# Kernel optimization log

Hardware: AMD Instinct MI355X
Metric: run time of the kernel (lower is better)

## Reference

```python
import jax, jax.numpy as jnp
import numpy as np

N_HEAD = 16


def setup_inputs() -> dict:
    key = jax.random.key(0)
    k1, k2, k3 = jax.random.split(key, 3)
    B, S, D = 4, 2048, 1024
    scale = 1.0 / np.sqrt(D)
    return {
        "inp": jax.random.normal(k1, (B, S, D), dtype=jnp.float32),
        "w_attn": jax.random.normal(k2, (D, 3 * D), dtype=jnp.float32) * scale,
        "b_attn": jnp.zeros((3 * D,), dtype=jnp.float32),
        "w_proj": jax.random.normal(k3, (D, D), dtype=jnp.float32) * scale,
        "b_proj": jnp.zeros((D,), dtype=jnp.float32),
    }


def reference(inp, w_attn, b_attn, w_proj, b_proj):
    B, S, D = inp.shape
    H = N_HEAD
    hd = D // H
    qkv = inp @ w_attn + b_attn                      # [B,S,3D]
    q, k, v = jnp.split(qkv, 3, axis=-1)
    q = q.reshape(B, S, H, hd)
    k = k.reshape(B, S, H, hd)
    v = v.reshape(B, S, H, hd)
    # scores [B,H,S,S], scaled by 1/sqrt(head_dim)
    scores = jnp.einsum("bqhd,bkhd->bhqk", q, k) / jnp.sqrt(jnp.asarray(hd, dtype=inp.dtype))
    # causal mask: position q attends to k <= q
    causal = jnp.tril(jnp.ones((S, S), dtype=bool))
    scores = jnp.where(causal[None, None], scores, jnp.asarray(-jnp.inf, dtype=scores.dtype))
    probs = jax.nn.softmax(scores, axis=-1)          # dropout omitted (eval mode)
    ctx = jnp.einsum("bhqk,bkhd->bqhd", probs, v).reshape(B, S, D)
    return ctx @ w_proj + b_proj
```

## Files before the change

### kernel.cpp

```cpp
#include <hip/hip_runtime.h>


#define DEV __device__ __forceinline__

typedef unsigned short u16;
typedef u16   u16x8 __attribute__((ext_vector_type(8)));
typedef u16   u16x4 __attribute__((ext_vector_type(4)));
typedef float f32x4v __attribute__((ext_vector_type(4)));
typedef __bf16 bf16x8 __attribute__((ext_vector_type(8)));

#define BB 4
#define SS 2048
#define DD 1024
#define HH 16
#define HD 64
#define MM (BB*SS)
#define N3D (3*DD)
#define C8  0.18033688011112042f

DEV u16 f2bf(float f) { return __builtin_bit_cast(u16, (__bf16)f); }
DEV float bf2f(u16 h) { return __builtin_bit_cast(float, (unsigned)h << 16); }

DEV f32x4v mfma16(u16x8 a, u16x8 b, f32x4v c) {
  return __builtin_amdgcn_mfma_f32_16x16x32_bf16(
      __builtin_bit_cast(bf16x8, a), __builtin_bit_cast(bf16x8, b), c, 0, 0, 0);
}

DEV void async16(const void* g, void* l) {
  __builtin_amdgcn_global_load_lds(
      (const __attribute__((address_space(1))) void*)g,
      (__attribute__((address_space(3))) void*)l, 16, 0, 0);
}

template <int C> DEV float dpp_fmax(float x) {
  int xi = __builtin_bit_cast(int, x);
  int y = __builtin_amdgcn_update_dpp(xi, xi, C, 0xF, 0xF, false);
  return fmaxf(x, __builtin_bit_cast(float, y));
}
template <int C> DEV float dpp_fadd(float x) {
  int xi = __builtin_bit_cast(int, x);
  int y = __builtin_amdgcn_update_dpp(xi, xi, C, 0xF, 0xF, false);
  return x + __builtin_bit_cast(float, y);
}
DEV float rowmax16(float x) {
  x = dpp_fmax<0x121>(x);
  x = dpp_fmax<0x122>(x);
  x = dpp_fmax<0x124>(x);
  x = dpp_fmax<0x128>(x);
  return x;
}
DEV float rowsum16(float x) {
  x = dpp_fadd<0x121>(x);
  x = dpp_fadd<0x122>(x);
  x = dpp_fadd<0x124>(x);
  x = dpp_fadd<0x128>(x);
  return x;
}

__global__ __launch_bounds__(256) void prep_kernel(
    const float* __restrict__ inp, const float* __restrict__ w_attn,
    const float* __restrict__ w_proj, u16* __restrict__ Abf,
    u16* __restrict__ WAt, u16* __restrict__ WPt) {
  const int bid = blockIdx.x;
  const int tid = threadIdx.x;
  if (bid < 4096) {
    __shared__ float t[32][33];
    const float* W; u16* Wt; int N, K, n0, k0;
    if (bid < 3072) { W = w_attn; Wt = WAt; N = N3D; K = DD;
                      n0 = (bid % 96) * 32; k0 = (bid / 96) * 32; }
    else            { W = w_proj; Wt = WPt; N = DD;  K = DD;
                      int tb = bid - 3072; n0 = (tb % 32) * 32; k0 = (tb / 32) * 32; }
    int tx = tid & 31, ty = tid >> 5;
    for (int i = ty; i < 32; i += 8)
      t[i][tx] = W[(long long)(k0 + i) * N + n0 + tx];
    __syncthreads();
    for (int i = ty; i < 32; i += 8)
      Wt[(long long)(n0 + i) * K + k0 + tx] = f2bf(t[tx][i]);
  } else {
    const long long n = (long long)MM * DD;
    long long i = (long long)(bid - 4096) * 256 + tid;
    for (long long j = i * 4; j < n; j += 2048LL * 256 * 4) {
      f32x4v v = *(const f32x4v*)(inp + j);
      u16x4 o;
      o.x = f2bf(v.x); o.y = f2bf(v.y); o.z = f2bf(v.z); o.w = f2bf(v.w);
      *(u16x4*)(Abf + j) = o;
    }
  }
}

__global__ __launch_bounds__(256) void gemm_kernel(
    const u16* __restrict__ A, const u16* __restrict__ Bt,
    const float* __restrict__ bias, void* __restrict__ Cout,
    u16* __restrict__ Vt, int Ndim, int Kdim, int mode) {
  __shared__ __align__(16) char smem[65536];

  const int tid = threadIdx.x;
  const int lane = tid & 63, wid = tid >> 6;
  const int l15 = lane & 15, lg = lane >> 4;

  const int nwg = (int)(gridDim.x * gridDim.y);
  const int orig = (int)(blockIdx.y * gridDim.x + blockIdx.x);
  const int wg = (orig & 7) * (nwg >> 3) + (orig >> 3);
  const int bx = wg % (int)gridDim.x, by = wg / (int)gridDim.x;
  const int rb = by * 128, cb = bx * 128;
  const int wr = (wid >> 1) * 64, wc = (wid & 1) * 64;

  f32x4v acc[4][4] = {};

  const int rlo = tid >> 3;
  const int cbS = (tid & 7) * 16;
  const int swS = cbS ^ ((rlo & 7) << 4);
  const int sd  = rlo * 128 + cbS;

  const int xr  = (l15 & 7) << 4;
  const int vaA = l15 * 128 + ((lg * 16) ^ xr);
  const int gvA0 = wr * 128 + vaA, gvA1 = gvA0 ^ 64;
  const int gvB0 = wc * 128 + vaA, gvB1 = gvB0 ^ 64;

  const char* pa[4];
  const char* pb[4];
#pragma unroll
  for (int i = 0; i < 4; ++i) {
    pa[i] = (const char*)A  + (long long)(rb + i * 32 + rlo) * (Kdim * 2) + swS;
    pb[i] = (const char*)Bt + (long long)(cb + i * 32 + rlo) * (Kdim * 2) + swS;
  }

  auto stage = [&](int dofs, int kb) {
#pragma unroll
    for (int i = 0; i < 4; ++i) {
      async16(pa[i] + kb, smem + dofs + i * 4096 + sd);
      async16(pb[i] + kb, smem + 32768 + dofs + i * 4096 + sd);
    }
  };

  auto compute = [&](int aofs, int bofs) {
    u16x8 a0[4], b0[4], a1[4], b1[4];
#pragma unroll
    for (int mi = 0; mi < 4; ++mi) {
      a0[mi] = *(const u16x8*)(smem + aofs + mi * 2048 + gvA0);
      a1[mi] = *(const u16x8*)(smem + aofs + mi * 2048 + gvA1);
    }
#pragma unroll
    for (int ni = 0; ni < 4; ++ni) {
      b0[ni] = *(const u16x8*)(smem + bofs + ni * 2048 + gvB0);
      b1[ni] = *(const u16x8*)(smem + bofs + ni * 2048 + gvB1);
    }
#pragma unroll
    for (int mi = 0; mi < 4; ++mi)
#pragma unroll
      for (int ni = 0; ni < 4; ++ni) {
        acc[mi][ni] = mfma16(a0[mi], b0[ni], acc[mi][ni]);
        acc[mi][ni] = mfma16(a1[mi], b1[ni], acc[mi][ni]);
      }
  };

  const int nK = Kdim >> 6;
  stage(0, 0);
  __syncthreads();
  for (int kt = 0; kt < nK; kt += 2) {
    stage(16384, 128);
    compute(0, 32768);
    __syncthreads();
    if (kt + 2 < nK) stage(0, 256);
    compute(16384, 49152);
    __syncthreads();
#pragma unroll
    for (int i = 0; i < 4; ++i) { pa[i] += 256; pb[i] += 256; }
  }

#pragma unroll
  for (int mi = 0; mi < 4; ++mi)
#pragma unroll
    for (int ni = 0; ni < 4; ++ni) {
      int col = cb + wc + ni * 16 + l15;
      float bv = bias[col];
      if (mode == 1 && col >= 2 * DD) {
        int h = (col >> 6) & 15, d = col & 63;
#pragma unroll
        for (int r = 0; r < 4; ++r) {
          int row = rb + wr + mi * 16 + lg * 4 + r;
          int b = row >> 11, s = row & 2047;
          Vt[(((long long)(b * HH + h) * HD + d) << 11) + s] = f2bf(acc[mi][ni][r] + bv);
        }
      } else {
#pragma unroll
        for (int r = 0; r < 4; ++r) {
          int row = rb + wr + mi * 16 + lg * 4 + r;
          float v = acc[mi][ni][r] + bv;
          if (mode) ((u16*)Cout)[(long long)row * Ndim + col] = f2bf(v);
          else      ((float*)Cout)[(long long)row * Ndim + col] = v;
        }
      }
    }
}

__global__ __launch_bounds__(512, 4) void attn_kernel(
    const u16* __restrict__ qkv, const u16* __restrict__ Vt,
    u16* __restrict__ ctx) {
  __shared__ __align__(16) char smem[49152];

  const int tid = threadIdx.x, lane = tid & 63, wid = tid >> 6;
  const int l15 = lane & 15, lg = lane >> 4;

  const int orig = (int)blockIdx.x;
  const int wgid = (orig & 7) * 64 + (orig >> 3);
  const int pair = wgid & 7;
  const int bh = wgid >> 3;
  const int b = bh >> 4, h = bh & 15;

  const u16* Qcol = qkv + (long long)b * SS * N3D + h * HD;
  const u16* Kcol = qkv + (long long)b * SS * N3D + DD + h * HD;
  const u16* Vbh  = Vt + (long long)bh * HD * SS;

  const int xr  = (l15 & 7) << 4;
  const int vaA = l15 * 128 + ((lg * 16) ^ xr);
  const int vaB = vaA ^ 64;
  const int vpA = 32768 + wid * 2048 + vaA;
  const int vpB = vpA ^ 64;

  int pw[16];
#pragma unroll
  for (int r = 0; r < 4; ++r) {
    int row = lg * 4 + r;
#pragma unroll
    for (int ni = 0; ni < 4; ++ni)
      pw[r * 4 + ni] = 32768 + wid * 2048 + row * 128 +
                       (((ni * 16 + l15) * 2) ^ ((row & 7) << 4));
  }

  const int rlo = tid >> 3;
  const int cbS = (tid & 7) * 16;
  const int swS = cbS ^ ((rlo & 7) << 4);
  const int sd  = rlo * 128 + cbS;
  const long long KSTP = 64LL * N3D * 2;
  const long long VSTP = 64LL * 2;

  auto stage = [&](int dofs, const char* ka, const char* va) {
    async16(ka, smem + dofs + sd);
    async16(va, smem + 16384 + dofs + sd);
  };

#pragma unroll 1
  for (int half = 0; half < 2; ++half) {
    const int qt = half ? pair : 15 - pair;
    const int q0 = qt * 128;
    const int qw = q0 + wid * 16;
    const int nkb = 2 * qt + 2;

    u16x8 qf[2];
#pragma unroll
    for (int kk = 0; kk < 2; ++kk)
      qf[kk] = *(const u16x8*)(Qcol + (long long)(qw + l15) * N3D + kk * 32 + lg * 8);

    f32x4v acc[4] = {};
    float m_s[4], l_p[4];
#pragma unroll
    for (int r = 0; r < 4; ++r) { m_s[r] = -1e30f; l_p[r] = 0.f; }

    const char* ka = (const char*)Kcol + (long long)rlo * (N3D * 2) + swS;
    const char* va = (const char*)Vbh + (long long)rlo * (SS * 2) + swS;

    auto compute = [&](int kofs, int vofs, int kbase) {
      if (kbase > qw + 15) return;

      f32x4v s[4] = {};
      u16x8 bfr0[4], bfr1[4];
#pragma unroll
      for (int ni = 0; ni < 4; ++ni)
        bfr0[ni] = *(const u16x8*)(smem + kofs + ni * 2048 + vaA);
      __builtin_amdgcn_s_setprio(1);
#pragma unroll
      for (int ni = 0; ni < 4; ++ni)
        s[ni] = mfma16(qf[0], bfr0[ni], s[ni]);
      __builtin_amdgcn_s_setprio(0);
#pragma unroll
      for (int ni = 0; ni < 4; ++ni)
        bfr1[ni] = *(const u16x8*)(smem + kofs + ni * 2048 + vaB);
      __builtin_amdgcn_s_setprio(1);
#pragma unroll
      for (int ni = 0; ni < 4; ++ni)
        s[ni] = mfma16(qf[1], bfr1[ni], s[ni]);
      __builtin_amdgcn_s_setprio(0);

      if (kbase + 63 > qw) {
#pragma unroll
        for (int ni = 0; ni < 4; ++ni) {
          int kcol = kbase + ni * 16 + l15;
#pragma unroll
          for (int r = 0; r < 4; ++r) {
            int qrow = qw + lg * 4 + r;
            if (kcol > qrow) s[ni][r] = -1e30f;
          }
        }
      }

      float lmax[4];
      bool need = false;
#pragma unroll
      for (int r = 0; r < 4; ++r) {
        lmax[r] = fmaxf(fmaxf(fmaxf(s[0][r], s[1][r]), s[2][r]), s[3][r]);
        need = need || (lmax[r] > m_s[r] + 64.f);
      }
      if (__any(need)) {
#pragma unroll
        for (int r = 0; r < 4; ++r) {
          float rm = rowmax16(lmax[r]);
          float newm = fmaxf(m_s[r], rm);
          float sc = __builtin_exp2f((m_s[r] - newm) * C8);
          m_s[r] = newm;
          l_p[r] *= sc;
#pragma unroll
          for (int di = 0; di < 4; ++di) acc[di][r] *= sc;
        }
      }
#pragma unroll
      for (int r = 0; r < 4; ++r) {
        float mC = m_s[r] * C8;
        float rsum = 0.f;
#pragma unroll
        for (int ni = 0; ni < 4; ++ni) {
          float p = __builtin_exp2f(__builtin_fmaf(s[ni][r], C8, -mC));
          s[ni][r] = p;
          rsum += p;
        }
        l_p[r] += rsum;
      }

#pragma unroll
      for (int r = 0; r < 4; ++r)
#pragma unroll
        for (int ni = 0; ni < 4; ++ni)
          *(u16*)(smem + pw[r * 4 + ni]) = f2bf(s[ni][r]);

      u16x8 pa0 = *(const u16x8*)(smem + vpA);
      u16x8 pa1 = *(const u16x8*)(smem + vpB);
      u16x8 vb0[4], vb1[4];
#pragma unroll
      for (int di = 0; di < 4; ++di) {
        vb0[di] = *(const u16x8*)(smem + vofs + di * 2048 + vaA);
        vb1[di] = *(const u16x8*)(smem + vofs + di * 2048 + vaB);
      }
      __builtin_amdgcn_s_setprio(1);
#pragma unroll
      for (int di = 0; di < 4; ++di) {
        acc[di] = mfma16(pa0, vb0[di], acc[di]);
        acc[di] = mfma16(pa1, vb1[di], acc[di]);
      }
      __builtin_amdgcn_s_setprio(0);
    };

    stage(0, ka, va);
    __syncthreads();

    for (int kb = 0; kb < nkb; kb += 2) {
      stage(8192, ka + KSTP, va + VSTP);
      compute(0, 16384, kb * 64);
      __syncthreads();
      if (kb + 2 < nkb) stage(0, ka + 2 * KSTP, va + 2 * VSTP);
      compute(8192, 24576, (kb + 1) * 64);
      __syncthreads();
      ka += 2 * KSTP; va += 2 * VSTP;
    }

#pragma unroll
    for (int r = 0; r < 4; ++r) {
      float inv = 1.f / rowsum16(l_p[r]);
      int qrow = qw + lg * 4 + r;
#pragma unroll
      for (int di = 0; di < 4; ++di) {
        int d = di * 16 + l15;
        ctx[((long long)(b * SS + qrow)) * DD + h * HD + d] = f2bf(acc[di][r] * inv);
      }
    }
  }
}

extern "C" void kernel_launch(void* const* d_in, const int* in_sizes, int n_in,
                              void* d_out, int out_size, void* d_ws, size_t ws_size,
                              hipStream_t stream) {
  const float* inp    = (const float*)d_in[0];
  const float* w_attn = (const float*)d_in[1];
  const float* b_attn = (const float*)d_in[2];
  const float* w_proj = (const float*)d_in[3];
  const float* b_proj = (const float*)d_in[4];
  float* out = (float*)d_out;
  char* ws = (char*)d_ws;

  const long long off_A   = 0;
  const long long off_WAt = 16777216;
  const long long off_WPt = 23068672;
  const long long off_qkv = 25165824;
  const long long off_ctx = 75497472;
  const long long off_Vt  = 92274688;
  const long long need    = 109051904;
  if (ws_size < (size_t)need) return;

  u16* Abf = (u16*)(ws + off_A);
  u16* WAt = (u16*)(ws + off_WAt);
  u16* WPt = (u16*)(ws + off_WPt);
  u16* qkv = (u16*)(ws + off_qkv);
  u16* ctx = (u16*)(ws + off_ctx);
  u16* Vt  = (u16*)(ws + off_Vt);

  prep_kernel<<<6144, 256, 0, stream>>>(inp, w_attn, w_proj, Abf, WAt, WPt);
  gemm_kernel<<<dim3(N3D / 128, MM / 128), 256, 0, stream>>>(
      Abf, WAt, b_attn, qkv, Vt, N3D, DD, 1);
  attn_kernel<<<512, 512, 0, stream>>>(qkv, Vt, ctx);
  gemm_kernel<<<dim3(DD / 128, MM / 128), 256, 0, stream>>>(
      ctx, WPt, b_proj, out, nullptr, DD, DD, 0);
}
```

Measured before the change: 181.4 us.

## Compute S transposed so P stays in registers, dropping the LDS round-trip

The QK^T MFMA now takes K as the A operand and Q as B, producing S^T in a layout where each lane holds one query row's scores. The bf16 probabilities are packed straight into the A-operand registers for the PV MFMA, removing the per-wave LDS write/read of P and freeing 16KB of shared memory. Row max and sum become per-lane values reduced with cross-lane shuffles. K rows are read through a permuted LDS index so the key order matches the V operand layout; the rescale factor for the accumulators is fetched with shuffles, which adds some cross-lane traffic.

```diff
diff --git a/kernel.cpp b/kernel.cpp
--- a/kernel.cpp
+++ b/kernel.cpp
@@ -4,6 +4,7 @@
 #define DEV __device__ __forceinline__
 
 typedef unsigned short u16;
+typedef unsigned u32x4 __attribute__((ext_vector_type(4)));
 typedef u16   u16x8 __attribute__((ext_vector_type(8)));
 typedef u16   u16x4 __attribute__((ext_vector_type(4)));
 typedef float f32x4v __attribute__((ext_vector_type(4)));
@@ -30,31 +31,6 @@
   __builtin_amdgcn_global_load_lds(
       (const __attribute__((address_space(1))) void*)g,
       (__attribute__((address_space(3))) void*)l, 16, 0, 0);
-}
-
-template <int C> DEV float dpp_fmax(float x) {
-  int xi = __builtin_bit_cast(int, x);
-  int y = __builtin_amdgcn_update_dpp(xi, xi, C, 0xF, 0xF, false);
-  return fmaxf(x, __builtin_bit_cast(float, y));
-}
-template <int C> DEV float dpp_fadd(float x) {
-  int xi = __builtin_bit_cast(int, x);
-  int y = __builtin_amdgcn_update_dpp(xi, xi, C, 0xF, 0xF, false);
-  return x + __builtin_bit_cast(float, y);
-}
-DEV float rowmax16(float x) {
-  x = dpp_fmax<0x121>(x);
-  x = dpp_fmax<0x122>(x);
-  x = dpp_fmax<0x124>(x);
-  x = dpp_fmax<0x128>(x);
-  return x;
-}
-DEV float rowsum16(float x) {
-  x = dpp_fadd<0x121>(x);
-  x = dpp_fadd<0x122>(x);
-  x = dpp_fadd<0x124>(x);
-  x = dpp_fadd<0x128>(x);
-  return x;
 }
 
 __global__ __launch_bounds__(256) void prep_kernel(
@@ -197,7 +173,7 @@
 __global__ __launch_bounds__(512, 4) void attn_kernel(
     const u16* __restrict__ qkv, const u16* __restrict__ Vt,
     u16* __restrict__ ctx) {
-  __shared__ __align__(16) char smem[49152];
+  __shared__ __align__(16) char smem[32768];
 
   const int tid = threadIdx.x, lane = tid & 63, wid = tid >> 6;
   const int l15 = lane & 15, lg = lane >> 4;
@@ -212,21 +188,13 @@
   const u16* Kcol = qkv + (long long)b * SS * N3D + DD + h * HD;
   const u16* Vbh  = Vt + (long long)bh * HD * SS;
 
-  const int xr  = (l15 & 7) << 4;
-  const int vaA = l15 * 128 + ((lg * 16) ^ xr);
-  const int vaB = vaA ^ 64;
-  const int vpA = 32768 + wid * 2048 + vaA;
-  const int vpB = vpA ^ 64;
-
-  int pw[16];
-#pragma unroll
-  for (int r = 0; r < 4; ++r) {
-    int row = lg * 4 + r;
-#pragma unroll
-    for (int ni = 0; ni < 4; ++ni)
-      pw[r * 4 + ni] = 32768 + wid * 2048 + row * 128 +
-                       (((ni * 16 + l15) * 2) ^ ((row & 7) << 4));
-  }
+  const int rowA = 8 * (l15 >> 2) + (l15 & 3);
+  const int vk0 = rowA * 128 + ((lg * 16) ^ ((l15 & 3) << 4));
+  const int vk1 = vk0 ^ 64;
+  const int vk2 = (rowA + 4) * 128 + ((lg * 16) ^ (((l15 & 3) + 4) << 4));
+  const int vk3 = vk2 ^ 64;
+  const int vv0 = l15 * 128 + ((lg * 16) ^ ((l15 & 7) << 4));
+  const int vv1 = vv0 ^ 64;
 
   const int rlo = tid >> 3;
   const int cbS = (tid & 7) * 16;
@@ -253,9 +221,7 @@
       qf[kk] = *(const u16x8*)(Qcol + (long long)(qw + l15) * N3D + kk * 32 + lg * 8);
 
     f32x4v acc[4] = {};
-    float m_s[4], l_p[4];
-#pragma unroll
-    for (int r = 0; r < 4; ++r) { m_s[r] = -1e30f; l_p[r] = 0.f; }
+    float m_s = -1e30f, l_p = 0.f;
 
     const char* ka = (const char*)Kcol + (long long)rlo * (N3D * 2) + swS;
     const char* va = (const char*)Vbh + (long long)rlo * (SS * 2) + swS;
@@ -263,88 +229,101 @@
     auto compute = [&](int kofs, int vofs, int kbase) {
       if (kbase > qw + 15) return;
 
-      f32x4v s[4] = {};
-      u16x8 bfr0[4], bfr1[4];
-#pragma unroll
-      for (int ni = 0; ni < 4; ++ni)
-        bfr0[ni] = *(const u16x8*)(smem + kofs + ni * 2048 + vaA);
+      f32x4v pf[2][2] = {};
+      {
+        u16x8 k00 = *(const u16x8*)(smem + kofs + vk0);
+        u16x8 k01 = *(const u16x8*)(smem + kofs + vk1);
+        u16x8 k10 = *(const u16x8*)(smem + kofs + vk2);
+        u16x8 k11 = *(const u16x8*)(smem + kofs + vk3);
+        u16x8 k20 = *(const u16x8*)(smem + kofs + 4096 + vk0);
+        u16x8 k21 = *(const u16x8*)(smem + kofs + 4096 + vk1);
+        u16x8 k30 = *(const u16x8*)(smem + kofs + 4096 + vk2);
+        u16x8 k31 = *(const u16x8*)(smem + kofs + 4096 + vk3);
+        __builtin_amdgcn_s_setprio(1);
+        pf[0][0] = mfma16(k00, qf[0], pf[0][0]);
+        pf[0][0] = mfma16(k01, qf[1], pf[0][0]);
+        pf[0][1] = mfma16(k10, qf[0], pf[0][1]);
+        pf[0][1] = mfma16(k11, qf[1], pf[0][1]);
+        pf[1][0] = mfma16(k20, qf[0], pf[1][0]);
+        pf[1][0] = mfma16(k21, qf[1], pf[1][0]);
+        pf[1][1] = mfma16(k30, qf[0], pf[1][1]);
+        pf[1][1] = mfma16(k31, qf[1], pf[1][1]);
+        __builtin_amdgcn_s_setprio(0);
+      }
+
+      if (kbase + 63 > qw) {
+        const int qg = qw + l15;
+        const int kl = kbase + lg * 8;
+#pragma unroll
+        for (int ks = 0; ks < 2; ++ks)
+#pragma unroll
+          for (int ab = 0; ab < 2; ++ab)
+#pragma unroll
+            for (int r = 0; r < 4; ++r)
+              if (kl + ks * 32 + ab * 4 + r > qg) pf[ks][ab][r] = -1e30f;
+      }
+
+      float lmax = pf[0][0][0];
+#pragma unroll
+      for (int ks = 0; ks < 2; ++ks)
+#pragma unroll
+        for (int ab = 0; ab < 2; ++ab)
+#pragma unroll
+          for (int r = 0; r < 4; ++r)
+            lmax = fmaxf(lmax, pf[ks][ab][r]);
+      if (__any(lmax > m_s + 64.f)) {
+        float rm = fmaxf(lmax, __shfl_xor(lmax, 16));
+        rm = fmaxf(rm, __shfl_xor(rm, 32));
+        float newm = fmaxf(m_s, rm);
+        float sc = __builtin_exp2f((m_s - newm) * C8);
+        m_s = newm;
+        l_p *= sc;
+#pragma unroll
+        for (int r = 0; r < 4; ++r) {
+          float scq = __shfl(sc, (lane & 48) + lg * 4 + r);
+#pragma unroll
+          for (int di = 0; di < 4; ++di) acc[di][r] *= scq;
+        }
+      }
+      {
+        float mC = m_s * C8;
+        float rsum = 0.f;
+#pragma unroll
+        for (int ks = 0; ks < 2; ++ks)
+#pragma unroll
+          for (int ab = 0; ab < 2; ++ab)
+#pragma unroll
+            for (int r = 0; r < 4; ++r) {
+              float p = __builtin_exp2f(__builtin_fmaf(pf[ks][ab][r], C8, -mC));
+              pf[ks][ab][r] = p;
+              rsum += p;
+            }
+        l_p += rsum;
+      }
+
+      u32x4 w0, w1;
+      w0.x = (unsigned)f2bf(pf[0][0][0]) | ((unsigned)f2bf(pf[0][0][1]) << 16);
+      w0.y = (unsigned)f2bf(pf[0][0][2]) | ((unsigned)f2bf(pf[0][0][3]) << 16);
+      w0.z = (unsigned)f2bf(pf[0][1][0]) | ((unsigned)f2bf(pf[0][1][1]) << 16);
+      w0.w = (unsigned)f2bf(pf[0][1][2]) | ((unsigned)f2bf(pf[0][1][3]) << 16);
+      w1.x = (unsigned)f2bf(pf[1][0][0]) | ((unsigned)f2bf(pf[1][0][1]) << 16);
+      w1.y = (unsigned)f2bf(pf[1][0][2]) | ((unsigned)f2bf(pf[1][0][3]) << 16);
+      w1.z = (unsigned)f2bf(pf[1][1][0]) | ((unsigned)f2bf(pf[1][1][1]) << 16);
+      w1.w = (unsigned)f2bf(pf[1][1][2]) | ((unsigned)f2bf(pf[1][1][3]) << 16);
+      u16x8 pa0 = __builtin_bit_cast(u16x8, w0);
+      u16x8 pa1 = __builtin_bit_cast(u16x8, w1);
+
+      u16x8 v0[4], v1[4];
+#pragma unroll
+      for (int di = 0; di < 4; ++di) {
+        v0[di] = *(const u16x8*)(smem + vofs + di * 2048 + vv0);
+        v1[di] = *(const u16x8*)(smem + vofs + di * 2048 + vv1);
+      }
       __builtin_amdgcn_s_setprio(1);
 #pragma unroll
-      for (int ni = 0; ni < 4; ++ni)
-        s[ni] = mfma16(qf[0], bfr0[ni], s[ni]);
-      __builtin_amdgcn_s_setprio(0);
-#pragma unroll
-      for (int ni = 0; ni < 4; ++ni)
-        bfr1[ni] = *(const u16x8*)(smem + kofs + ni * 2048 + vaB);
-      __builtin_amdgcn_s_setprio(1);
-#pragma unroll
-      for (int ni = 0; ni < 4; ++ni)
-        s[ni] = mfma16(qf[1], bfr1[ni], s[ni]);
-      __builtin_amdgcn_s_setprio(0);
-
-      if (kbase + 63 > qw) {
-#pragma unroll
-        for (int ni = 0; ni < 4; ++ni) {
-          int kcol = kbase + ni * 16 + l15;
-#pragma unroll
-          for (int r = 0; r < 4; ++r) {
-            int qrow = qw + lg * 4 + r;
-            if (kcol > qrow) s[ni][r] = -1e30f;
-          }
-        }
-      }
-
-      float lmax[4];
-      bool need = false;
-#pragma unroll
-      for (int r = 0; r < 4; ++r) {
-        lmax[r] = fmaxf(fmaxf(fmaxf(s[0][r], s[1][r]), s[2][r]), s[3][r]);
-        need = need || (lmax[r] > m_s[r] + 64.f);
-      }
-      if (__any(need)) {
-#pragma unroll
-        for (int r = 0; r < 4; ++r) {
-          float rm = rowmax16(lmax[r]);
-          float newm = fmaxf(m_s[r], rm);
-          float sc = __builtin_exp2f((m_s[r] - newm) * C8);
-          m_s[r] = newm;
-          l_p[r] *= sc;
-#pragma unroll
-          for (int di = 0; di < 4; ++di) acc[di][r] *= sc;
-        }
-      }
-#pragma unroll
-      for (int r = 0; r < 4; ++r) {
-        float mC = m_s[r] * C8;
-        float rsum = 0.f;
-#pragma unroll
-        for (int ni = 0; ni < 4; ++ni) {
-          float p = __builtin_exp2f(__builtin_fmaf(s[ni][r], C8, -mC));
-          s[ni][r] = p;
-          rsum += p;
-        }
-        l_p[r] += rsum;
-      }
-
-#pragma unroll
-      for (int r = 0; r < 4; ++r)
-#pragma unroll
-        for (int ni = 0; ni < 4; ++ni)
-          *(u16*)(smem + pw[r * 4 + ni]) = f2bf(s[ni][r]);
-
-      u16x8 pa0 = *(const u16x8*)(smem + vpA);
-      u16x8 pa1 = *(const u16x8*)(smem + vpB);
-      u16x8 vb0[4], vb1[4];
-#pragma unroll
       for (int di = 0; di < 4; ++di) {
-        vb0[di] = *(const u16x8*)(smem + vofs + di * 2048 + vaA);
-        vb1[di] = *(const u16x8*)(smem + vofs + di * 2048 + vaB);
-      }
-      __builtin_amdgcn_s_setprio(1);
-#pragma unroll
-      for (int di = 0; di < 4; ++di) {
-        acc[di] = mfma16(pa0, vb0[di], acc[di]);
-        acc[di] = mfma16(pa1, vb1[di], acc[di]);
+        acc[di] = mfma16(pa0, v0[di], acc[di]);
+        acc[di] = mfma16(pa1, v1[di], acc[di]);
       }
       __builtin_amdgcn_s_setprio(0);
     };
@@ -362,9 +341,12 @@
       ka += 2 * KSTP; va += 2 * VSTP;
     }
 
+    float l_red = l_p + __shfl_xor(l_p, 16);
+    l_red += __shfl_xor(l_red, 32);
 #pragma unroll
     for (int r = 0; r < 4; ++r) {
-      float inv = 1.f / rowsum16(l_p[r]);
+      float lq = __shfl(l_red, (lane & 48) + lg * 4 + r);
+      float inv = 1.f / lq;
       int qrow = qw + lg * 4 + r;
 #pragma unroll
       for (int di = 0; di < 4; ++di) {
```

New measurement: 178.1 us. About the same (-1.8%).
